# Optimization experiments

Hardware: AMD Instinct MI355X
Metric: run time of the kernel (lower is better)

Reference implementation:

```python
import jax, jax.numpy as jnp
import numpy as np

D_MODEL, D_HEAD, N_HEADS = 1024, 64, 16
B, S = 2, 2048


def setup_inputs() -> dict:
    key = jax.random.key(0)
    ks = jax.random.split(key, 8)
    init = lambda k, shape: jax.random.normal(k, shape, dtype=jnp.float32) * (1.0 / np.sqrt(D_MODEL))
    return {
        "query": jax.random.normal(ks[0], (B, S, D_MODEL), dtype=jnp.float32),
        "key": jax.random.normal(ks[1], (B, S, D_MODEL), dtype=jnp.float32),
        "value": jax.random.normal(ks[2], (B, S, D_MODEL), dtype=jnp.float32),
        "W_Q": init(ks[3], (N_HEADS, D_MODEL, D_HEAD)),
        "W_K": init(ks[4], (N_HEADS, D_MODEL, D_HEAD)),
        "W_V": init(ks[5], (N_HEADS, D_MODEL, D_HEAD)),
        "W_O": init(ks[6], (N_HEADS, D_HEAD, D_MODEL)),
        "b_Q": jnp.zeros((N_HEADS, D_HEAD), dtype=jnp.float32),
        "b_K": jnp.zeros((N_HEADS, D_HEAD), dtype=jnp.float32),
        "b_V": jnp.zeros((N_HEADS, D_HEAD), dtype=jnp.float32),
        "b_O": jnp.zeros((D_MODEL,), dtype=jnp.float32),
    }


def reference(query, key, value, W_Q, W_K, W_V, W_O, b_Q, b_K, b_V, b_O):
    scale = jnp.asarray(np.sqrt(D_HEAD), dtype=query.dtype)
    # per-head linear projections: [B,S,D] x [H,D,K] -> [B,S,H,K]
    q = jnp.einsum('bsd,hdk->bshk', query, W_Q) + b_Q
    k = jnp.einsum('bsd,hdk->bshk', key, W_K) + b_K
    v = jnp.einsum('bsd,hdk->bshk', value, W_V) + b_V
    # full non-causal attention scores [B,H,Q,K]
    attn_score = jnp.einsum('bqhk,bshk->bhqs', q, k) / scale
    pattern = jax.nn.softmax(attn_score, axis=-1)
    pattern = jnp.where(jnp.isnan(pattern), jnp.zeros_like(pattern), pattern)
    # weighted sum of values -> [B,Q,H,K]
    z = jnp.einsum('bhqs,bshk->bqhk', pattern, v)
    # output projection: combine heads [B,Q,H,K] x [H,K,D] -> [B,Q,D]
    out = jnp.einsum('bqhk,hkd->bqd', z, W_O) + b_O
    return out
```

## Files before the change

kernel.cpp:

```cpp
#include <hip/hip_runtime.h>
#include <hip/hip_bf16.h>
#include <cstdint>

#define DM 1024
#define SEQ 2048

typedef __attribute__((ext_vector_type(4))) float f32x4;
typedef __attribute__((ext_vector_type(16))) float f32x16;
typedef __attribute__((ext_vector_type(8))) short s16x8;
typedef __attribute__((ext_vector_type(8))) __bf16 bf16x8;

__device__ inline unsigned short f2bf(float f) {
  union { float f; unsigned u; } x; x.f = f;
  return (unsigned short)((x.u + 0x7FFFu + ((x.u >> 16) & 1u)) >> 16);
}
__device__ inline float bf2f(unsigned short u) {
  union { unsigned u; float f; } x; x.u = ((unsigned)u) << 16; return x.f;
}
__device__ inline bf16x8 ld_frag(const void* p) {
  union { s16x8 s; bf16x8 b; } u; u.s = *(const s16x8*)p; return u.b;
}
__device__ inline bf16x8 mkfrag(unsigned w0, unsigned w1, unsigned w2, unsigned w3) {
  union { unsigned u[4]; bf16x8 v; } t; t.u[0]=w0; t.u[1]=w1; t.u[2]=w2; t.u[3]=w3; return t.v;
}
__device__ inline float fexp2(float x) {
#if __has_builtin(__builtin_amdgcn_exp2f)
  return __builtin_amdgcn_exp2f(x);
#else
  return exp2f(x);
#endif
}
__device__ inline unsigned cvtpk(float lo, float hi) {
  unsigned r; asm("v_cvt_pk_bf16_f32 %0, %1, %2" : "=v"(r) : "v"(lo), "v"(hi)); return r;
}
__device__ inline void plswap(unsigned &a, unsigned &b) {
#if __has_builtin(__builtin_amdgcn_permlane32_swap)
  auto r = __builtin_amdgcn_permlane32_swap(a, b, false, false);
  a = r[0]; b = r[1];
#else
  asm volatile("v_permlane32_swap_b32 %0, %1" : "+v"(a), "+v"(b));
#endif
}
__device__ inline void gl16(const void* g, void* l) {
  __builtin_amdgcn_global_load_lds(
      (const __attribute__((address_space(1))) void*)(uintptr_t)g,
      (__attribute__((address_space(3))) void*)(uint32_t)(uintptr_t)l, 16, 0, 0);
}
__device__ inline f32x16 zero16() {
  f32x16 r = {0.f,0.f,0.f,0.f,0.f,0.f,0.f,0.f,0.f,0.f,0.f,0.f,0.f,0.f,0.f,0.f};
  return r;
}

__global__ __launch_bounds__(256) void prep_x(
    const float* __restrict__ xq, const float* __restrict__ xk, const float* __restrict__ xv,
    unsigned short* __restrict__ Xq, unsigned short* __restrict__ Xk, unsigned short* __restrict__ Xv) {
  int task = blockIdx.y;
  const float* src = task == 0 ? xq : task == 1 ? xk : xv;
  unsigned short* dst = task == 0 ? Xq : task == 1 ? Xk : Xv;
  int g = blockIdx.x * 256 + threadIdx.x;
  const float4* s4 = (const float4*)src;
  float4 a = s4[g * 2], b = s4[g * 2 + 1];
  s16x8 o;
  o[0] = (short)f2bf(a.x); o[1] = (short)f2bf(a.y);
  o[2] = (short)f2bf(a.z); o[3] = (short)f2bf(a.w);
  o[4] = (short)f2bf(b.x); o[5] = (short)f2bf(b.y);
  o[6] = (short)f2bf(b.z); o[7] = (short)f2bf(b.w);
  *(s16x8*)&dst[g * 8] = o;
}

__global__ __launch_bounds__(256) void tr_wqkv(
    const float* __restrict__ wq, const float* __restrict__ wk, const float* __restrict__ wv,
    unsigned short* __restrict__ WtQ, unsigned short* __restrict__ WtK, unsigned short* __restrict__ WtV) {
  __shared__ float T[64][65];
  int z = blockIdx.z;
  const float* src = (z == 0 ? wq : z == 1 ? wk : wv) + blockIdx.y * 65536 + blockIdx.x * 64 * 64;
  unsigned short* dst = (z == 0 ? WtQ : z == 1 ? WtK : WtV) + blockIdx.y * 65536;
  int tid = threadIdx.x, r0 = blockIdx.x * 64;
#pragma unroll
  for (int i = 0; i < 16; ++i) {
    int idx = tid + i * 256; int r = idx >> 6, cc = idx & 63;
    T[r][cc] = src[r * 64 + cc];
  }
  __syncthreads();
#pragma unroll
  for (int i = 0; i < 16; ++i) {
    int idx = tid + i * 256; int cc = idx >> 6, r = idx & 63;
    dst[cc * 1024 + r0 + r] = f2bf(T[r][cc]);
  }
}

__global__ __launch_bounds__(256) void tr_wo(const float* __restrict__ wo, unsigned short* __restrict__ WtO) {
  __shared__ float T[64][65];
  int r0 = blockIdx.x * 64, c0 = blockIdx.y * 64;
  int tid = threadIdx.x;
#pragma unroll
  for (int i = 0; i < 16; ++i) {
    int idx = tid + i * 256; int r = idx >> 6, cc = idx & 63;
    T[r][cc] = wo[(size_t)(r0 + r) * 1024 + c0 + cc];
  }
  __syncthreads();
#pragma unroll
  for (int i = 0; i < 16; ++i) {
    int idx = tid + i * 256; int cc = idx >> 6, r = idx & 63;
    WtO[(size_t)(c0 + cc) * 1024 + r0 + r] = f2bf(T[r][cc]);
  }
}

__global__ __launch_bounds__(256) void tr_v(const unsigned short* __restrict__ vb, unsigned short* __restrict__ vT) {
  __shared__ float T[64][65];
  int st = blockIdx.x, h = blockIdx.y, b = blockIdx.z;
  const unsigned short* src = vb + ((size_t)(b * SEQ + st * 64)) * DM + h * 64;
  unsigned short* dst = vT + ((size_t)(b * 16 + h)) * 64 * SEQ + st * 64;
  int tid = threadIdx.x;
#pragma unroll
  for (int i = 0; i < 16; ++i) {
    int idx = tid + i * 256; int r = idx >> 6, cc = idx & 63;
    T[r][cc] = bf2f(src[(size_t)r * DM + cc]);
  }
  __syncthreads();
#pragma unroll
  for (int i = 0; i < 16; ++i) {
    int idx = tid + i * 256; int cc = idx >> 6, r = idx & 63;
    dst[(size_t)cc * SEQ + r] = f2bf(T[r][cc]);
  }
}

template<int F32OUT>
__device__ inline void gemm_core(const unsigned short* __restrict__ A,
                                 const unsigned short* __restrict__ Bt,
                                 const float* __restrict__ bias, void* __restrict__ C,
                                 float scale, int row0, int col0,
                                 unsigned short* As, unsigned short* Bs) {
  int tid = threadIdx.x;
  int w = tid >> 6, l = tid & 63;
  int wr = w >> 1, wc = w & 1;
  int c = l & 15, gg = l >> 4;
  f32x4 acc[4][4] = {};
  for (int k0 = 0; k0 < 1024; k0 += 32) {
    __syncthreads();
    {
      int ch = tid;
#pragma unroll
      for (int i = 0; i < 2; ++i, ch += 256) {
        gl16(&A[(size_t)(row0 + (ch >> 2)) * 1024 + k0 + (ch & 3) * 8], &As[ch * 8]);
        gl16(&Bt[(size_t)(col0 + (ch >> 2)) * 1024 + k0 + (ch & 3) * 8], &Bs[ch * 8]);
      }
    }
    asm volatile("s_waitcnt vmcnt(0)" ::: "memory");
    __syncthreads();
    bf16x8 af[4], bfv[4];
#pragma unroll
    for (int mt = 0; mt < 4; ++mt) af[mt] = ld_frag(&As[(wr * 64 + mt * 16 + c) * 32 + gg * 8]);
#pragma unroll
    for (int nt = 0; nt < 4; ++nt) bfv[nt] = ld_frag(&Bs[(wc * 64 + nt * 16 + c) * 32 + gg * 8]);
#pragma unroll
    for (int mt = 0; mt < 4; ++mt)
#pragma unroll
      for (int nt = 0; nt < 4; ++nt)
        acc[mt][nt] = __builtin_amdgcn_mfma_f32_16x16x32_bf16(af[mt], bfv[nt], acc[mt][nt], 0, 0, 0);
  }
#pragma unroll
  for (int mt = 0; mt < 4; ++mt)
#pragma unroll
    for (int nt = 0; nt < 4; ++nt)
#pragma unroll
      for (int r = 0; r < 4; ++r) {
        int row = row0 + wr * 64 + mt * 16 + gg * 4 + r;
        int col = col0 + wc * 64 + nt * 16 + c;
        float vv = (acc[mt][nt][r] + bias[col]) * scale;
        if (F32OUT) ((float*)C)[(size_t)row * 1024 + col] = vv;
        else        ((unsigned short*)C)[(size_t)row * 1024 + col] = f2bf(vv);
      }
}

__global__ __launch_bounds__(256) void gemm_proj(
    const unsigned short* __restrict__ Xq, const unsigned short* __restrict__ Xk,
    const unsigned short* __restrict__ Xv,
    const unsigned short* __restrict__ WtQ, const unsigned short* __restrict__ WtK,
    const unsigned short* __restrict__ WtV,
    const float* __restrict__ bQ, const float* __restrict__ bK, const float* __restrict__ bV,
    unsigned short* __restrict__ qb, unsigned short* __restrict__ kb, unsigned short* __restrict__ vb,
    float scaleQ) {
  __shared__ unsigned short As[4096], Bs[4096];
  int id = blockIdx.x + blockIdx.y * 32;
  id = (id & 7) * 32 + (id >> 3);
  int row0 = (id & 31) * 128, col0 = (id >> 5) * 128;
  int z = blockIdx.z;
  const unsigned short* A  = z == 0 ? Xq : z == 1 ? Xk : Xv;
  const unsigned short* Bt = z == 0 ? WtQ : z == 1 ? WtK : WtV;
  const float* bias        = z == 0 ? bQ : z == 1 ? bK : bV;
  unsigned short* C        = z == 0 ? qb : z == 1 ? kb : vb;
  float scale = z == 0 ? scaleQ : 1.f;
  gemm_core<0>(A, Bt, bias, C, scale, row0, col0, As, Bs);
}

__global__ __launch_bounds__(256) void gemm_out(
    const unsigned short* __restrict__ zb, const unsigned short* __restrict__ WtO,
    const float* __restrict__ bO, float* __restrict__ out) {
  __shared__ unsigned short As[4096], Bs[4096];
  int id = blockIdx.x + blockIdx.y * 32;
  id = (id & 7) * 32 + (id >> 3);
  int row0 = (id & 31) * 128, col0 = (id >> 5) * 128;
  gemm_core<1>(zb, WtO, bO, out, 1.f, row0, col0, As, Bs);
}

__global__ __launch_bounds__(256) void attn_kernel(
    const unsigned short* __restrict__ q, const unsigned short* __restrict__ k,
    const unsigned short* __restrict__ vt, unsigned short* __restrict__ z) {
  __shared__ unsigned short SM[8192];
  unsigned short* Ks = SM;
  unsigned short* Vs = SM + 4096;
  int tid = threadIdx.x, w = tid >> 6, l = tid & 63;
  int l5 = l & 31, hi = l >> 5;
  int id = blockIdx.x + blockIdx.y * 16;
  id = (id & 7) * 64 + (id >> 3);
  int qt = id & 15, bh = id >> 4;
  int b = bh >> 4, h = bh & 15;
  int q0 = qt * 128 + w * 32;

  const unsigned short* kbh = k + ((size_t)b * SEQ) * DM + h * 64;
  const unsigned short* vbh = vt + ((size_t)bh) * 64 * SEQ;

  bf16x8 qf[4];
  {
    size_t qbase = ((size_t)(b * SEQ + q0 + l5)) * DM + h * 64 + hi * 8;
#pragma unroll
    for (int kk = 0; kk < 4; ++kk) qf[kk] = ld_frag(&q[qbase + kk * 16]);
  }

  f32x16 o0 = zero16(), o1 = zero16();
  float m = -1e30f, lsum = 0.f;

  for (int kv0 = 0; kv0 < SEQ; kv0 += 64) {
    __syncthreads();
#pragma unroll
    for (int i = 0; i < 2; ++i) {
      int ch = tid + i * 256;
      int kv = ch >> 3, cc = ch & 7;
      gl16(&kbh[(size_t)(kv0 + kv) * DM + ((cc ^ (kv & 7)) * 8)], &Ks[ch * 8]);
    }
#pragma unroll
    for (int i = 0; i < 2; ++i) {
      int ch = tid + i * 256;
      int d = ch >> 3, cc = ch & 7;
      gl16(&vbh[(size_t)d * SEQ + kv0 + ((cc ^ (d & 7)) * 8)], &Vs[ch * 8]);
    }
    asm volatile("s_waitcnt vmcnt(0)" ::: "memory");
    __syncthreads();

    f32x16 st0 = zero16(), st1 = zero16();
#pragma unroll
    for (int kk = 0; kk < 4; ++kk) {
      int sw = ((kk * 2 + hi) ^ (l5 & 7)) * 8;
      bf16x8 ka0 = ld_frag(&Ks[l5 * 64 + sw]);
      bf16x8 ka1 = ld_frag(&Ks[(32 + l5) * 64 + sw]);
      st0 = __builtin_amdgcn_mfma_f32_32x32x16_bf16(ka0, qf[kk], st0, 0, 0, 0);
      st1 = __builtin_amdgcn_mfma_f32_32x32x16_bf16(ka1, qf[kk], st1, 0, 0, 0);
    }

    float pm = st0[0];
#pragma unroll
    for (int r = 1; r < 16; ++r) pm = fmaxf(pm, st0[r]);
#pragma unroll
    for (int r = 0; r < 16; ++r) pm = fmaxf(pm, st1[r]);
    pm = fmaxf(pm, __shfl_xor(pm, 32));
    if (__any(pm > m + 8.f)) {
      float mn = fmaxf(m, pm);
      float fac = fexp2(m - mn);
      m = mn;
      lsum *= fac;
#pragma unroll
      for (int r = 0; r < 16; ++r) { o0[r] *= fac; o1[r] *= fac; }
    }
    float ps = 0.f;
#pragma unroll
    for (int r = 0; r < 16; ++r) { float p = fexp2(st0[r] - m); st0[r] = p; ps += p; }
#pragma unroll
    for (int r = 0; r < 16; ++r) { float p = fexp2(st1[r] - m); st1[r] = p; ps += p; }
    ps += __shfl_xor(ps, 32);
    lsum += ps;

    unsigned A1 = cvtpk(st0[0], st0[1]),   B1 = cvtpk(st0[4], st0[5]);
    unsigned A2 = cvtpk(st0[2], st0[3]),   B2 = cvtpk(st0[6], st0[7]);
    plswap(A1, B1); plswap(A2, B2);
    bf16x8 pf0 = mkfrag(A1, A2, B1, B2);
    unsigned A3 = cvtpk(st0[8], st0[9]),   B3 = cvtpk(st0[12], st0[13]);
    unsigned A4 = cvtpk(st0[10], st0[11]), B4 = cvtpk(st0[14], st0[15]);
    plswap(A3, B3); plswap(A4, B4);
    bf16x8 pf1 = mkfrag(A3, A4, B3, B4);
    unsigned A5 = cvtpk(st1[0], st1[1]),   B5 = cvtpk(st1[4], st1[5]);
    unsigned A6 = cvtpk(st1[2], st1[3]),   B6 = cvtpk(st1[6], st1[7]);
    plswap(A5, B5); plswap(A6, B6);
    bf16x8 pf2 = mkfrag(A5, A6, B5, B6);
    unsigned A7 = cvtpk(st1[8], st1[9]),   B7 = cvtpk(st1[12], st1[13]);
    unsigned A8 = cvtpk(st1[10], st1[11]), B8 = cvtpk(st1[14], st1[15]);
    plswap(A7, B7); plswap(A8, B8);
    bf16x8 pf3 = mkfrag(A7, A8, B7, B8);

#pragma unroll
    for (int kk = 0; kk < 4; ++kk) {
      int sw = ((kk * 2 + hi) ^ (l5 & 7)) * 8;
      bf16x8 va0 = ld_frag(&Vs[l5 * 64 + sw]);
      bf16x8 va1 = ld_frag(&Vs[(32 + l5) * 64 + sw]);
      bf16x8 pcur = kk == 0 ? pf0 : kk == 1 ? pf1 : kk == 2 ? pf2 : pf3;
      o0 = __builtin_amdgcn_mfma_f32_32x32x16_bf16(va0, pcur, o0, 0, 0, 0);
      o1 = __builtin_amdgcn_mfma_f32_32x32x16_bf16(va1, pcur, o1, 0, 0, 0);
    }
  }

  __syncthreads();
  float inv = 1.f / lsum;
  char* Twc = (char*)(SM + w * 2048);
#pragma unroll
  for (int g = 0; g < 4; ++g)
#pragma unroll
    for (int j = 0; j < 2; ++j) {
      int d = g * 8 + 4 * hi + 2 * j;
      unsigned w0 = cvtpk(o0[g * 4 + 2 * j] * inv, o0[g * 4 + 2 * j + 1] * inv);
      *(unsigned*)(Twc + ((l5 * 128 + d * 2) ^ ((l5 & 7) << 4))) = w0;
      unsigned w1 = cvtpk(o1[g * 4 + 2 * j] * inv, o1[g * 4 + 2 * j + 1] * inv);
      *(unsigned*)(Twc + ((l5 * 128 + (d + 32) * 2) ^ ((l5 & 7) << 4))) = w1;
    }
  asm volatile("s_waitcnt lgkmcnt(0)" ::: "memory");
  int qs = l >> 1, half = l & 1;
  size_t zbase = ((size_t)(b * SEQ + q0 + qs)) * DM + h * 64 + half * 32;
#pragma unroll
  for (int j = 0; j < 4; ++j) {
    int off = (qs * 128 + half * 64 + j * 16) ^ ((qs & 7) << 4);
    *(s16x8*)&z[zbase + j * 8] = *(const s16x8*)(Twc + off);
  }
}

extern "C" void kernel_launch(void* const* d_in, const int* in_sizes, int n_in,
                              void* d_out, int out_size, void* d_ws, size_t ws_size,
                              hipStream_t stream) {
  const float* query = (const float*)d_in[0];
  const float* key_  = (const float*)d_in[1];
  const float* value = (const float*)d_in[2];
  const float* W_Q = (const float*)d_in[3];
  const float* W_K = (const float*)d_in[4];
  const float* W_V = (const float*)d_in[5];
  const float* W_O = (const float*)d_in[6];
  const float* b_Q = (const float*)d_in[7];
  const float* b_K = (const float*)d_in[8];
  const float* b_V = (const float*)d_in[9];
  const float* b_O = (const float*)d_in[10];

  char* ws = (char*)d_ws;
  const size_t MB = 1024 * 1024;
  unsigned short* Xq  = (unsigned short*)(ws + 0);
  unsigned short* Xk  = (unsigned short*)(ws + 8 * MB);
  unsigned short* Xv  = (unsigned short*)(ws + 16 * MB);
  unsigned short* WtQ = (unsigned short*)(ws + 24 * MB);
  unsigned short* WtK = (unsigned short*)(ws + 26 * MB);
  unsigned short* WtV = (unsigned short*)(ws + 28 * MB);
  unsigned short* WtO = (unsigned short*)(ws + 30 * MB);
  unsigned short* qb  = (unsigned short*)(ws + 32 * MB);
  unsigned short* kb  = (unsigned short*)(ws + 40 * MB);
  unsigned short* vb  = (unsigned short*)(ws + 48 * MB);
  unsigned short* vT  = Xk;
  unsigned short* zb  = Xq;

  const float SCALE_Q = 0.18033688011112043f;

  prep_x<<<dim3(2048, 3), 256, 0, stream>>>(query, key_, value, Xq, Xk, Xv);
  tr_wqkv<<<dim3(16, 16, 3), 256, 0, stream>>>(W_Q, W_K, W_V, WtQ, WtK, WtV);
  tr_wo<<<dim3(16, 16), 256, 0, stream>>>(W_O, WtO);
  gemm_proj<<<dim3(32, 8, 3), 256, 0, stream>>>(Xq, Xk, Xv, WtQ, WtK, WtV,
                                                b_Q, b_K, b_V, qb, kb, vb, SCALE_Q);
  tr_v<<<dim3(32, 16, 2), 256, 0, stream>>>(vb, vT);
  attn_kernel<<<dim3(16, 32), 256, 0, stream>>>(qb, kb, vT, zb);
  gemm_out<<<dim3(32, 8), 256, 0, stream>>>(zb, WtO, b_O, (float*)d_out);
}
```

Measured before the change: 239.2 us.

## Multi-buffer GEMM and attention loads, merge weight/input prep kernels

Both the GEMM core and the attention kernel now keep a 4-slot LDS ring of tiles. Loads run two tiles ahead using async global-to-LDS copies, with partial vmcnt waits and a single barrier per iteration, instead of a full drain and two syncthreads per tile. Attention also loads Q through LDS, and it raises wave priority around the MFMA blocks. The three preprocessing kernels (input bf16 cast, QKV weight transpose, W_O transpose) are merged into one launch. The aim is to hide global memory latency and cut launch overhead. The cost is much larger LDS use per block (64KB for the GEMMs, 80KB for attention), which can limit occupancy.

```diff
diff --git a/kernel.cpp b/kernel.cpp
--- a/kernel.cpp
+++ b/kernel.cpp
@@ -51,58 +51,61 @@
   return r;
 }
 
-__global__ __launch_bounds__(256) void prep_x(
+__global__ __launch_bounds__(256) void prep_all(
     const float* __restrict__ xq, const float* __restrict__ xk, const float* __restrict__ xv,
-    unsigned short* __restrict__ Xq, unsigned short* __restrict__ Xk, unsigned short* __restrict__ Xv) {
-  int task = blockIdx.y;
-  const float* src = task == 0 ? xq : task == 1 ? xk : xv;
-  unsigned short* dst = task == 0 ? Xq : task == 1 ? Xk : Xv;
-  int g = blockIdx.x * 256 + threadIdx.x;
-  const float4* s4 = (const float4*)src;
-  float4 a = s4[g * 2], b = s4[g * 2 + 1];
-  s16x8 o;
-  o[0] = (short)f2bf(a.x); o[1] = (short)f2bf(a.y);
-  o[2] = (short)f2bf(a.z); o[3] = (short)f2bf(a.w);
-  o[4] = (short)f2bf(b.x); o[5] = (short)f2bf(b.y);
-  o[6] = (short)f2bf(b.z); o[7] = (short)f2bf(b.w);
-  *(s16x8*)&dst[g * 8] = o;
-}
-
-__global__ __launch_bounds__(256) void tr_wqkv(
     const float* __restrict__ wq, const float* __restrict__ wk, const float* __restrict__ wv,
-    unsigned short* __restrict__ WtQ, unsigned short* __restrict__ WtK, unsigned short* __restrict__ WtV) {
+    const float* __restrict__ wo,
+    unsigned short* __restrict__ Xq, unsigned short* __restrict__ Xk, unsigned short* __restrict__ Xv,
+    unsigned short* __restrict__ WtQ, unsigned short* __restrict__ WtK, unsigned short* __restrict__ WtV,
+    unsigned short* __restrict__ WtO) {
   __shared__ float T[64][65];
-  int z = blockIdx.z;
-  const float* src = (z == 0 ? wq : z == 1 ? wk : wv) + blockIdx.y * 65536 + blockIdx.x * 64 * 64;
-  unsigned short* dst = (z == 0 ? WtQ : z == 1 ? WtK : WtV) + blockIdx.y * 65536;
-  int tid = threadIdx.x, r0 = blockIdx.x * 64;
-#pragma unroll
-  for (int i = 0; i < 16; ++i) {
-    int idx = tid + i * 256; int r = idx >> 6, cc = idx & 63;
-    T[r][cc] = src[r * 64 + cc];
-  }
-  __syncthreads();
-#pragma unroll
-  for (int i = 0; i < 16; ++i) {
-    int idx = tid + i * 256; int cc = idx >> 6, r = idx & 63;
-    dst[cc * 1024 + r0 + r] = f2bf(T[r][cc]);
-  }
-}
-
-__global__ __launch_bounds__(256) void tr_wo(const float* __restrict__ wo, unsigned short* __restrict__ WtO) {
-  __shared__ float T[64][65];
-  int r0 = blockIdx.x * 64, c0 = blockIdx.y * 64;
-  int tid = threadIdx.x;
-#pragma unroll
-  for (int i = 0; i < 16; ++i) {
-    int idx = tid + i * 256; int r = idx >> 6, cc = idx & 63;
-    T[r][cc] = wo[(size_t)(r0 + r) * 1024 + c0 + cc];
-  }
-  __syncthreads();
-#pragma unroll
-  for (int i = 0; i < 16; ++i) {
-    int idx = tid + i * 256; int cc = idx >> 6, r = idx & 63;
-    WtO[(size_t)(c0 + cc) * 1024 + r0 + r] = f2bf(T[r][cc]);
+  int bid = blockIdx.x, tid = threadIdx.x;
+  if (bid < 6144) {
+    int task = bid >> 11;
+    const float* src = task == 0 ? xq : task == 1 ? xk : xv;
+    unsigned short* dst = task == 0 ? Xq : task == 1 ? Xk : Xv;
+    int g = (bid & 2047) * 256 + tid;
+    const float4* s4 = (const float4*)src;
+    float4 a = s4[g * 2], b = s4[g * 2 + 1];
+    s16x8 o;
+    o[0] = (short)f2bf(a.x); o[1] = (short)f2bf(a.y);
+    o[2] = (short)f2bf(a.z); o[3] = (short)f2bf(a.w);
+    o[4] = (short)f2bf(b.x); o[5] = (short)f2bf(b.y);
+    o[6] = (short)f2bf(b.z); o[7] = (short)f2bf(b.w);
+    *(s16x8*)&dst[g * 8] = o;
+  } else if (bid < 6912) {
+    int idx = bid - 6144;
+    int zz = idx >> 8, rem = idx & 255;
+    int by = rem >> 4, bx = rem & 15;
+    const float* src = (zz == 0 ? wq : zz == 1 ? wk : wv) + by * 65536 + bx * 64 * 64;
+    unsigned short* dst = (zz == 0 ? WtQ : zz == 1 ? WtK : WtV) + by * 65536;
+    int r0 = bx * 64;
+#pragma unroll
+    for (int i = 0; i < 16; ++i) {
+      int idx2 = tid + i * 256; int r = idx2 >> 6, cc = idx2 & 63;
+      T[r][cc] = src[r * 64 + cc];
+    }
+    __syncthreads();
+#pragma unroll
+    for (int i = 0; i < 16; ++i) {
+      int idx2 = tid + i * 256; int cc = idx2 >> 6, r = idx2 & 63;
+      dst[cc * 1024 + r0 + r] = f2bf(T[r][cc]);
+    }
+  } else {
+    int idx = bid - 6912;
+    int bx = idx & 15, by = idx >> 4;
+    int r0 = bx * 64, c0 = by * 64;
+#pragma unroll
+    for (int i = 0; i < 16; ++i) {
+      int idx2 = tid + i * 256; int r = idx2 >> 6, cc = idx2 & 63;
+      T[r][cc] = wo[(size_t)(r0 + r) * 1024 + c0 + cc];
+    }
+    __syncthreads();
+#pragma unroll
+    for (int i = 0; i < 16; ++i) {
+      int idx2 = tid + i * 256; int cc = idx2 >> 6, r = idx2 & 63;
+      WtO[(size_t)(c0 + cc) * 1024 + r0 + r] = f2bf(T[r][cc]);
+    }
   }
 }
 
@@ -130,24 +133,33 @@
                                  const unsigned short* __restrict__ Bt,
                                  const float* __restrict__ bias, void* __restrict__ C,
                                  float scale, int row0, int col0,
-                                 unsigned short* As, unsigned short* Bs) {
+                                 unsigned short* GS) {
   int tid = threadIdx.x;
   int w = tid >> 6, l = tid & 63;
   int wr = w >> 1, wc = w & 1;
   int c = l & 15, gg = l >> 4;
+  auto STAGE = [&](int buf, int k0) {
+    unsigned short* As = GS + buf * 8192;
+    unsigned short* Bs = As + 4096;
+#pragma unroll
+    for (int i = 0; i < 2; ++i) {
+      int ch = tid + i * 256;
+      gl16(&A[(size_t)(row0 + (ch >> 2)) * 1024 + k0 + (ch & 3) * 8], &As[ch * 8]);
+      gl16(&Bt[(size_t)(col0 + (ch >> 2)) * 1024 + k0 + (ch & 3) * 8], &Bs[ch * 8]);
+    }
+  };
   f32x4 acc[4][4] = {};
-  for (int k0 = 0; k0 < 1024; k0 += 32) {
-    __syncthreads();
-    {
-      int ch = tid;
-#pragma unroll
-      for (int i = 0; i < 2; ++i, ch += 256) {
-        gl16(&A[(size_t)(row0 + (ch >> 2)) * 1024 + k0 + (ch & 3) * 8], &As[ch * 8]);
-        gl16(&Bt[(size_t)(col0 + (ch >> 2)) * 1024 + k0 + (ch & 3) * 8], &Bs[ch * 8]);
-      }
-    }
-    asm volatile("s_waitcnt vmcnt(0)" ::: "memory");
-    __syncthreads();
+  STAGE(0, 0);
+  STAGE(1, 32);
+  for (int kt = 0; kt < 32; ++kt) {
+    if (kt < 30) STAGE((kt + 2) & 3, (kt + 2) * 32);
+    if (kt < 30)      asm volatile("s_waitcnt vmcnt(8)" ::: "memory");
+    else if (kt==30)  asm volatile("s_waitcnt vmcnt(4)" ::: "memory");
+    else              asm volatile("s_waitcnt vmcnt(0)" ::: "memory");
+    __builtin_amdgcn_s_barrier();
+    __builtin_amdgcn_sched_barrier(0);
+    const unsigned short* As = GS + (kt & 3) * 8192;
+    const unsigned short* Bs = As + 4096;
     bf16x8 af[4], bfv[4];
 #pragma unroll
     for (int mt = 0; mt < 4; ++mt) af[mt] = ld_frag(&As[(wr * 64 + mt * 16 + c) * 32 + gg * 8]);
@@ -181,7 +193,7 @@
     const float* __restrict__ bQ, const float* __restrict__ bK, const float* __restrict__ bV,
     unsigned short* __restrict__ qb, unsigned short* __restrict__ kb, unsigned short* __restrict__ vb,
     float scaleQ) {
-  __shared__ unsigned short As[4096], Bs[4096];
+  __shared__ unsigned short GS[32768];
   int id = blockIdx.x + blockIdx.y * 32;
   id = (id & 7) * 32 + (id >> 3);
   int row0 = (id & 31) * 128, col0 = (id >> 5) * 128;
@@ -191,64 +203,86 @@
   const float* bias        = z == 0 ? bQ : z == 1 ? bK : bV;
   unsigned short* C        = z == 0 ? qb : z == 1 ? kb : vb;
   float scale = z == 0 ? scaleQ : 1.f;
-  gemm_core<0>(A, Bt, bias, C, scale, row0, col0, As, Bs);
+  gemm_core<0>(A, Bt, bias, C, scale, row0, col0, GS);
 }
 
 __global__ __launch_bounds__(256) void gemm_out(
     const unsigned short* __restrict__ zb, const unsigned short* __restrict__ WtO,
     const float* __restrict__ bO, float* __restrict__ out) {
-  __shared__ unsigned short As[4096], Bs[4096];
+  __shared__ unsigned short GS[32768];
   int id = blockIdx.x + blockIdx.y * 32;
   id = (id & 7) * 32 + (id >> 3);
   int row0 = (id & 31) * 128, col0 = (id >> 5) * 128;
-  gemm_core<1>(zb, WtO, bO, out, 1.f, row0, col0, As, Bs);
+  gemm_core<1>(zb, WtO, bO, out, 1.f, row0, col0, GS);
 }
 
 __global__ __launch_bounds__(256) void attn_kernel(
     const unsigned short* __restrict__ q, const unsigned short* __restrict__ k,
     const unsigned short* __restrict__ vt, unsigned short* __restrict__ z) {
-  __shared__ unsigned short SM[8192];
-  unsigned short* Ks = SM;
-  unsigned short* Vs = SM + 4096;
+  __shared__ unsigned short SM[40960];
   int tid = threadIdx.x, w = tid >> 6, l = tid & 63;
   int l5 = l & 31, hi = l >> 5;
   int id = blockIdx.x + blockIdx.y * 16;
   id = (id & 7) * 64 + (id >> 3);
   int qt = id & 15, bh = id >> 4;
   int b = bh >> 4, h = bh & 15;
-  int q0 = qt * 128 + w * 32;
+  int q0 = qt * 128;
 
   const unsigned short* kbh = k + ((size_t)b * SEQ) * DM + h * 64;
   const unsigned short* vbh = vt + ((size_t)bh) * 64 * SEQ;
-
-  bf16x8 qf[4];
-  {
-    size_t qbase = ((size_t)(b * SEQ + q0 + l5)) * DM + h * 64 + hi * 8;
-#pragma unroll
-    for (int kk = 0; kk < 4; ++kk) qf[kk] = ld_frag(&q[qbase + kk * 16]);
-  }
-
-  f32x16 o0 = zero16(), o1 = zero16();
-  float m = -1e30f, lsum = 0.f;
-
-  for (int kv0 = 0; kv0 < SEQ; kv0 += 64) {
-    __syncthreads();
+  const unsigned short* qbh = q + ((size_t)(b * SEQ + q0)) * DM + h * 64;
+  unsigned short* Qs = SM + 32768;
+
+#pragma unroll
+  for (int i = 0; i < 4; ++i) {
+    int ch = tid + i * 256;
+    int row = ch >> 3, cc = ch & 7;
+    gl16(&qbh[(size_t)row * DM + ((cc ^ (row & 7)) * 8)], &Qs[ch * 8]);
+  }
+  auto STAGE = [&](int buf, int kv0) {
+    unsigned short* Kd = SM + buf * 8192;
+    unsigned short* Vd = Kd + 4096;
 #pragma unroll
     for (int i = 0; i < 2; ++i) {
       int ch = tid + i * 256;
       int kv = ch >> 3, cc = ch & 7;
-      gl16(&kbh[(size_t)(kv0 + kv) * DM + ((cc ^ (kv & 7)) * 8)], &Ks[ch * 8]);
+      gl16(&kbh[(size_t)(kv0 + kv) * DM + ((cc ^ (kv & 7)) * 8)], &Kd[ch * 8]);
     }
 #pragma unroll
     for (int i = 0; i < 2; ++i) {
       int ch = tid + i * 256;
       int d = ch >> 3, cc = ch & 7;
-      gl16(&vbh[(size_t)d * SEQ + kv0 + ((cc ^ (d & 7)) * 8)], &Vs[ch * 8]);
-    }
-    asm volatile("s_waitcnt vmcnt(0)" ::: "memory");
-    __syncthreads();
+      gl16(&vbh[(size_t)d * SEQ + kv0 + ((cc ^ (d & 7)) * 8)], &Vd[ch * 8]);
+    }
+  };
+  STAGE(0, 0);
+  STAGE(1, 64);
+  asm volatile("s_waitcnt vmcnt(8)" ::: "memory");
+  __builtin_amdgcn_s_barrier();
+  __builtin_amdgcn_sched_barrier(0);
+
+  bf16x8 qf[4];
+#pragma unroll
+  for (int kk = 0; kk < 4; ++kk) {
+    int x = kk * 2 + hi;
+    qf[kk] = ld_frag(&Qs[(w * 32 + l5) * 64 + ((x ^ (l5 & 7)) * 8)]);
+  }
+
+  f32x16 o0 = zero16(), o1 = zero16();
+  float m = -1e30f, lsum = 0.f;
+
+  for (int kt = 0; kt < 32; ++kt) {
+    if (kt < 30) STAGE((kt + 2) & 3, (kt + 2) * 64);
+    if (kt < 30)      asm volatile("s_waitcnt vmcnt(8)" ::: "memory");
+    else if (kt==30)  asm volatile("s_waitcnt vmcnt(4)" ::: "memory");
+    else              asm volatile("s_waitcnt vmcnt(0)" ::: "memory");
+    __builtin_amdgcn_s_barrier();
+    __builtin_amdgcn_sched_barrier(0);
+    const unsigned short* Ks = SM + (kt & 3) * 8192;
+    const unsigned short* Vs = Ks + 4096;
 
     f32x16 st0 = zero16(), st1 = zero16();
+    __builtin_amdgcn_s_setprio(1);
 #pragma unroll
     for (int kk = 0; kk < 4; ++kk) {
       int sw = ((kk * 2 + hi) ^ (l5 & 7)) * 8;
@@ -257,6 +291,7 @@
       st0 = __builtin_amdgcn_mfma_f32_32x32x16_bf16(ka0, qf[kk], st0, 0, 0, 0);
       st1 = __builtin_amdgcn_mfma_f32_32x32x16_bf16(ka1, qf[kk], st1, 0, 0, 0);
     }
+    __builtin_amdgcn_s_setprio(0);
 
     float pm = st0[0];
 #pragma unroll
@@ -297,6 +332,7 @@
     plswap(A7, B7); plswap(A8, B8);
     bf16x8 pf3 = mkfrag(A7, A8, B7, B8);
 
+    __builtin_amdgcn_s_setprio(1);
 #pragma unroll
     for (int kk = 0; kk < 4; ++kk) {
       int sw = ((kk * 2 + hi) ^ (l5 & 7)) * 8;
@@ -306,9 +342,10 @@
       o0 = __builtin_amdgcn_mfma_f32_32x32x16_bf16(va0, pcur, o0, 0, 0, 0);
       o1 = __builtin_amdgcn_mfma_f32_32x32x16_bf16(va1, pcur, o1, 0, 0, 0);
     }
-  }
-
-  __syncthreads();
+    __builtin_amdgcn_s_setprio(0);
+  }
+
+  __builtin_amdgcn_s_barrier();
   float inv = 1.f / lsum;
   char* Twc = (char*)(SM + w * 2048);
 #pragma unroll
@@ -323,7 +360,7 @@
     }
   asm volatile("s_waitcnt lgkmcnt(0)" ::: "memory");
   int qs = l >> 1, half = l & 1;
-  size_t zbase = ((size_t)(b * SEQ + q0 + qs)) * DM + h * 64 + half * 32;
+  size_t zbase = ((size_t)(b * SEQ + q0 + w * 32 + qs)) * DM + h * 64 + half * 32;
 #pragma unroll
   for (int j = 0; j < 4; ++j) {
     int off = (qs * 128 + half * 64 + j * 16) ^ ((qs & 7) << 4);
@@ -363,9 +400,8 @@
 
   const float SCALE_Q = 0.18033688011112043f;
 
-  prep_x<<<dim3(2048, 3), 256, 0, stream>>>(query, key_, value, Xq, Xk, Xv);
-  tr_wqkv<<<dim3(16, 16, 3), 256, 0, stream>>>(W_Q, W_K, W_V, WtQ, WtK, WtV);
-  tr_wo<<<dim3(16, 16), 256, 0, stream>>>(W_O, WtO);
+  prep_all<<<dim3(7168), 256, 0, stream>>>(query, key_, value, W_Q, W_K, W_V, W_O,
+                                           Xq, Xk, Xv, WtQ, WtK, WtV, WtO);
   gemm_proj<<<dim3(32, 8, 3), 256, 0, stream>>>(Xq, Xk, Xv, WtQ, WtK, WtV,
                                                 b_Q, b_K, b_V, qb, kb, vb, SCALE_Q);
   tr_v<<<dim3(32, 16, 2), 256, 0, stream>>>(vb, vT);
```

Result: faster. 231.6 us (-3.2%).
